# Kernel optimization log

Hardware: AMD Instinct MI355X
Metric: run time of the kernel (lower is better)

## Reference

```python
import jax, jax.numpy as jnp
import numpy as np

T, B, IN, HID, OUT = 512, 2048, 28, 198, 10

def setup_inputs() -> dict:
    key = jax.random.key(0)
    ks = jax.random.split(key, 6)
    s = 1.0 / np.sqrt(HID)
    return {
        "x": jax.random.normal(ks[0], (T, B, IN), dtype=jnp.float32),
        "H": jax.random.normal(ks[1], (HID, HID), dtype=jnp.float32) * s,
        "U": jax.random.normal(ks[2], (IN, HID), dtype=jnp.float32) * s,
        "A": jax.random.normal(ks[3], (OUT, HID), dtype=jnp.float32) * s,
        "b": jax.random.normal(ks[4], (HID,), dtype=jnp.float32) * 0.1,
        "c": jax.random.normal(ks[5], (OUT,), dtype=jnp.float32) * 0.1,
    }

def reference(x, H, U, A, b, c):
    # Precompute input projections for all timesteps in one big GEMM:
    # [T,B,IN] @ [IN,HID] -> [T,B,HID]
    xu = jnp.einsum('tbi,ih->tbh', x, U) + b

    def step(h, xu_t):
        h = jnp.tanh(h @ H.T + xu_t)
        return h, None

    h0 = jnp.zeros((x.shape[1], H.shape[0]), dtype=x.dtype)
    h, _ = jax.lax.scan(step, h0, xu)
    return h @ A.T + c
```

## Files before the change

### kernel.cpp

```cpp
#include <hip/hip_runtime.h>


#define T_STEPS 512
#define BATCH   2048
#define IN_DIM  28
#define HID     198
#define OUT_DIM 10
#define BB      8
#define NTAU    4
#define NTHREADS 1024

typedef __attribute__((ext_vector_type(8))) _Float16 half8;
typedef __attribute__((ext_vector_type(4))) float   floatx4;

__device__ __forceinline__ floatx4 mfma16(half8 a, half8 b, floatx4 c) {
    return __builtin_amdgcn_mfma_f32_16x16x32_f16(a, b, c, 0, 0, 0);
}

__device__ __forceinline__ float fast_tanh(float x) {
    float e = __builtin_amdgcn_exp2f(x * 2.885390081777926357f);
    float r = __builtin_amdgcn_rcpf(e + 1.0f);
    return __builtin_fmaf(-2.0f, r, 1.0f);
}

__device__ __forceinline__ float ror8(float v) {
    return __builtin_bit_cast(float,
        __builtin_amdgcn_mov_dpp(__builtin_bit_cast(int, v),
                                 0x128 , 0xf, 0xf, true));
}

__global__ void __launch_bounds__(NTHREADS, 4)
rnn_kernel(const float* __restrict__ x, const float* __restrict__ H,
           const float* __restrict__ U, const float* __restrict__ A,
           const float* __restrict__ bvec, const float* __restrict__ cvec,
           float* __restrict__ out)
{
    __shared__ __align__(16) _Float16 lds_A[2][NTAU][64][8];
    __shared__ float lds_h[BB][204];

    const int tid  = threadIdx.x;
    const int lane = tid & 63;
    const int wv   = tid >> 6;
    const int n16  = lane & 15;
    const int q    = lane >> 4;
    const int b0   = blockIdx.x * BB;

    {
        _Float16* p0 = &lds_A[0][0][0][0];
        for (int i = tid; i < 2*NTAU*64*8; i += NTHREADS) p0[i] = (_Float16)0.0f;
    }

    const floatx4 zero4 = {0.0f, 0.0f, 0.0f, 0.0f};
    const bool is_cw = (wv < 13);

    const int aslot = lane;

    const int jbase0 = wv*16;
    const int jbase1 = wv*16 + 8;
    const bool g1_on = is_cw && (jbase1 < HID);
    const int jl = n16 & 7;
    const int j0 = jbase0 + jl;
    const int j1 = jbase1 + jl;
    const int b_lane = 2*q + (n16 >> 3);

    half8 Bf0[NTAU], Bf1[NTAU];
    float bias0 = 0.0f, bias1 = 0.0f;
    if (is_cw) {
        bias0 = (n16 < 8 && j0 < HID) ? bvec[j0] : 0.0f;
        bias1 = (n16 < 8 && g1_on)    ? bvec[j1] : 0.0f;
        #pragma unroll
        for (int tau = 0; tau < NTAU; ++tau) {
            half8 f0, f1;
            #pragma unroll
            for (int i = 0; i < 8; ++i) {
                const int k = tau*64 + (n16 >> 3)*32 + q*8 + i;
                float v0 = 0.0f, v1 = 0.0f;
                if (j0 < HID) {
                    if (k < HID)                          v0 = H[j0*HID + k];
                    else if (k >= 224 && k < 224+IN_DIM)  v0 = U[(k-224)*HID + j0];
                }
                if (g1_on) {
                    if (k < HID)                          v1 = H[j1*HID + k];
                    else if (k >= 224 && k < 224+IN_DIM)  v1 = U[(k-224)*HID + j1];
                }
                f0[i] = (_Float16)v0;
                f1[i] = (_Float16)v1;
            }
            Bf0[tau] = f0; Bf1[tau] = f1;
        }
    }

    const int e0_tau  = j0 >> 6;
    const int e0_slot = ((j0 >> 3) & 3)*16 + (b_lane >> 1)*4 + (b_lane & 1)*2
                      + ((j0 >> 5) & 1);
    const int e0_idx  = j0 & 7;
    const int e1_tau  = j1 >> 6;
    const int e1_slot = ((j1 >> 3) & 3)*16 + (b_lane >> 1)*4 + (b_lane & 1)*2
                      + ((j1 >> 5) & 1);
    const int e1_idx  = j1 & 7;

    const int srow = lane & 31, sq = srow >> 3, sr8 = srow & 7;
    const int sslot = sq*16 + (sr8 >> 1)*4 + (sr8 & 1)*2 + 1;
    const float* xrow_s = x + (size_t)(b0 + sr8) * IN_DIM + sq*8;
    const size_t tstride = (size_t)BATCH * IN_DIM;
    floatx4 sA0 = zero4, sA1 = zero4, sB0 = zero4, sB1 = zero4;

    auto issueLd = [&](int tn, floatx4& f0, floatx4& f1) {
        const float* p = xrow_s + (size_t)tn * tstride;
        f0 = *(const floatx4*)p;
        f1 = (sq < 3) ? *(const floatx4*)(p + 4) : zero4;
    };
    auto commitX = [&](floatx4 f0, floatx4 f1, int buf) {
        half8 ax;
        ax[0] = (_Float16)f0[0]; ax[1] = (_Float16)f0[1];
        ax[2] = (_Float16)f0[2]; ax[3] = (_Float16)f0[3];
        ax[4] = (_Float16)f1[0]; ax[5] = (_Float16)f1[1];
        ax[6] = (_Float16)f1[2]; ax[7] = (_Float16)f1[3];
        *(half8*)&lds_A[buf][3][sslot][0] = ax;
    };

    __syncthreads();

    if (wv == 15 && lane < 32) {
        floatx4 t0, t1;
        issueLd(0, t0, t1);
        issueLd(1, sA0, sA1);
        issueLd(2, sB0, sB1);
        commitX(t0, t1, 0);
    }

    auto computeStep = [&](int rb, int wb, bool last) {
        if (!is_cw) return;
        floatx4 a0 = {bias0, bias0, bias0, bias0};
        floatx4 a1 = {bias1, bias1, bias1, bias1};
        #pragma unroll
        for (int tau = 0; tau < NTAU; ++tau) {
            const half8 av = *(const half8*)&lds_A[rb][tau][aslot][0];
            a0 = mfma16(av, Bf0[tau], a0);
            if (g1_on) a1 = mfma16(av, Bf1[tau], a1);
        }
        const float send0 = (n16 < 8) ? a0[2] : a0[1];
        const float send1 = (n16 < 8) ? a1[2] : a1[1];
        const float recv0 = ror8(send0);
        const float recv1 = ror8(send1);
        const float s0 = ((n16 < 8) ? a0[0] : a0[3]) + recv0;
        const float s1 = ((n16 < 8) ? a1[0] : a1[3]) + recv1;
        if (j0 < HID) {
            const float v = fast_tanh(s0);
            lds_A[wb][e0_tau][e0_slot][e0_idx] = (_Float16)v;
            if (last) lds_h[b_lane][j0] = v;
        }
        if (g1_on) {
            const float v = fast_tanh(s1);
            lds_A[wb][e1_tau][e1_slot][e1_idx] = (_Float16)v;
            if (last) lds_h[b_lane][j1] = v;
        }
    };

    #pragma unroll 1
    for (int t = 0; t < T_STEPS; t += 2) {
        __syncthreads();
        if (wv == 15 && lane < 32) {
            commitX(sA0, sA1, 1);
            const int tn = (t+3 < T_STEPS) ? (t+3) : (T_STEPS-1);
            issueLd(tn, sA0, sA1);
        }
        computeStep(0, 1, false);

        __syncthreads();
        if (wv == 15 && lane < 32) {
            commitX(sB0, sB1, 0);
            const int tn = (t+4 < T_STEPS) ? (t+4) : (T_STEPS-1);
            issueLd(tn, sB0, sB1);
        }
        computeStep(1, 0, (t + 2) == T_STEPS);
    }

    __syncthreads();

    if (tid < BB * OUT_DIM) {
        const int r = tid / OUT_DIM;
        const int o = tid % OUT_DIM;
        float s = cvec[o];
        for (int k = 0; k < HID; ++k) s += lds_h[r][k] * A[o*HID + k];
        out[(size_t)(b0 + r) * OUT_DIM + o] = s;
    }
}

extern "C" void kernel_launch(void* const* d_in, const int* in_sizes, int n_in,
                              void* d_out, int out_size, void* d_ws, size_t ws_size,
                              hipStream_t stream) {
    const float* x  = (const float*)d_in[0];
    const float* H  = (const float*)d_in[1];
    const float* U  = (const float*)d_in[2];
    const float* A  = (const float*)d_in[3];
    const float* b  = (const float*)d_in[4];
    const float* c  = (const float*)d_in[5];
    float* out = (float*)d_out;

    rnn_kernel<<<dim3(BATCH / BB), dim3(NTHREADS), 0, stream>>>(x, H, U, A, b, c, out);
}
```

Before: 405.0 us.

## Halve batch tile to 4 rows and spread 3-4 column groups per wave

Each block now handles 4 batch rows with 512 threads instead of 8 rows with 1024. Seven compute waves each own 3 or 4 column groups of 8 and reuse one set of LDS A-fragment loads across those groups. The shared-memory activation layout is shrunk to 32 slots, so half of each MFMA's rows are padding. This doubles the grid to 512 blocks and cuts barrier participants per recurrence step, at the cost of a longer serial MFMA chain per wave and more registers for weights.

```diff
diff --git a/kernel.cpp b/kernel.cpp
--- a/kernel.cpp
+++ b/kernel.cpp
@@ -6,9 +6,10 @@
 #define IN_DIM  28
 #define HID     198
 #define OUT_DIM 10
-#define BB      8
+#define BB      4
 #define NTAU    4
-#define NTHREADS 1024
+#define NTHREADS 512
+#define NGMAX   4
 
 typedef __attribute__((ext_vector_type(8))) _Float16 half8;
 typedef __attribute__((ext_vector_type(4))) float   floatx4;
@@ -35,7 +36,7 @@
            const float* __restrict__ bvec, const float* __restrict__ cvec,
            float* __restrict__ out)
 {
-    __shared__ __align__(16) _Float16 lds_A[2][NTAU][64][8];
+    __shared__ __align__(16) _Float16 lds_A[2][NTAU][32][8];
     __shared__ float lds_h[BB][204];
 
     const int tid  = threadIdx.x;
@@ -43,72 +44,68 @@
     const int wv   = tid >> 6;
     const int n16  = lane & 15;
     const int q    = lane >> 4;
+    const int jl   = n16 & 7;
     const int b0   = blockIdx.x * BB;
 
     {
         _Float16* p0 = &lds_A[0][0][0][0];
-        for (int i = tid; i < 2*NTAU*64*8; i += NTHREADS) p0[i] = (_Float16)0.0f;
+        for (int i = tid; i < 2*NTAU*32*8; i += NTHREADS) p0[i] = (_Float16)0.0f;
     }
 
     const floatx4 zero4 = {0.0f, 0.0f, 0.0f, 0.0f};
-    const bool is_cw = (wv < 13);
+    const bool is_cw = (wv < 7);
 
-    const int aslot = lane;
+    const int aslot = q*8 + (n16 & 7);
 
-    const int jbase0 = wv*16;
-    const int jbase1 = wv*16 + 8;
-    const bool g1_on = is_cw && (jbase1 < HID);
-    const int jl = n16 & 7;
-    const int j0 = jbase0 + jl;
-    const int j1 = jbase1 + jl;
-    const int b_lane = 2*q + (n16 >> 3);
+    const int ng    = (wv < 4) ? 4 : 3;
+    const int gbase = (wv < 4) ? 4*wv : 16 + 3*(wv - 4);
 
-    half8 Bf0[NTAU], Bf1[NTAU];
-    float bias0 = 0.0f, bias1 = 0.0f;
+    const int b_lane = (2*q + (n16 >> 3)) & 3;
+
+    half8 Bf[NGMAX][NTAU];
+    float bias[NGMAX];
+    int   eoff[NGMAX];
+    int   jcol[NGMAX];
     if (is_cw) {
-        bias0 = (n16 < 8 && j0 < HID) ? bvec[j0] : 0.0f;
-        bias1 = (n16 < 8 && g1_on)    ? bvec[j1] : 0.0f;
         #pragma unroll
-        for (int tau = 0; tau < NTAU; ++tau) {
-            half8 f0, f1;
+        for (int g = 0; g < NGMAX; ++g) {
+            const int jbase = (gbase + g) * 8;
+            const int j = jbase + jl;
+            jcol[g] = j;
+            const bool act = (g < ng) && (j < HID);
+            bias[g] = act ? bvec[j] : 0.0f;
+            eoff[g] = (j >> 6)*256
+                    + ((((j >> 3) & 3)*8) + b_lane*2 + ((j >> 5) & 1))*8
+                    + (j & 7);
             #pragma unroll
-            for (int i = 0; i < 8; ++i) {
-                const int k = tau*64 + (n16 >> 3)*32 + q*8 + i;
-                float v0 = 0.0f, v1 = 0.0f;
-                if (j0 < HID) {
-                    if (k < HID)                          v0 = H[j0*HID + k];
-                    else if (k >= 224 && k < 224+IN_DIM)  v0 = U[(k-224)*HID + j0];
+            for (int tau = 0; tau < NTAU; ++tau) {
+                half8 f;
+                #pragma unroll
+                for (int i = 0; i < 8; ++i) {
+                    const int k = tau*64 + (n16 >> 3)*32 + q*8 + i;
+                    float v = 0.0f;
+                    if (act) {
+                        if (k < HID)                          v = H[j*HID + k];
+                        else if (k >= 224 && k < 224+IN_DIM)  v = U[(k-224)*HID + j];
+                    }
+                    f[i] = (_Float16)v;
                 }
-                if (g1_on) {
-                    if (k < HID)                          v1 = H[j1*HID + k];
-                    else if (k >= 224 && k < 224+IN_DIM)  v1 = U[(k-224)*HID + j1];
-                }
-                f0[i] = (_Float16)v0;
-                f1[i] = (_Float16)v1;
+                Bf[g][tau] = f;
             }
-            Bf0[tau] = f0; Bf1[tau] = f1;
         }
     }
 
-    const int e0_tau  = j0 >> 6;
-    const int e0_slot = ((j0 >> 3) & 3)*16 + (b_lane >> 1)*4 + (b_lane & 1)*2
-                      + ((j0 >> 5) & 1);
-    const int e0_idx  = j0 & 7;
-    const int e1_tau  = j1 >> 6;
-    const int e1_slot = ((j1 >> 3) & 3)*16 + (b_lane >> 1)*4 + (b_lane & 1)*2
-                      + ((j1 >> 5) & 1);
-    const int e1_idx  = j1 & 7;
-
-    const int srow = lane & 31, sq = srow >> 3, sr8 = srow & 7;
-    const int sslot = sq*16 + (sr8 >> 1)*4 + (sr8 & 1)*2 + 1;
-    const float* xrow_s = x + (size_t)(b0 + sr8) * IN_DIM + sq*8;
+    const int sb  = (lane >> 2) & 3;
+    const int skq = lane & 3;
+    const int sslot = skq*8 + sb*2 + 1;
+    const float* xrow_s = x + (size_t)(b0 + sb) * IN_DIM + skq*8;
     const size_t tstride = (size_t)BATCH * IN_DIM;
     floatx4 sA0 = zero4, sA1 = zero4, sB0 = zero4, sB1 = zero4;
 
     auto issueLd = [&](int tn, floatx4& f0, floatx4& f1) {
         const float* p = xrow_s + (size_t)tn * tstride;
         f0 = *(const floatx4*)p;
-        f1 = (sq < 3) ? *(const floatx4*)(p + 4) : zero4;
+        f1 = (skq < 3) ? *(const floatx4*)(p + 4) : zero4;
     };
     auto commitX = [&](floatx4 f0, floatx4 f1, int buf) {
         half8 ax;
@@ -121,7 +118,7 @@
 
     __syncthreads();
 
-    if (wv == 15 && lane < 32) {
+    if (wv == 7 && lane < 16) {
         floatx4 t0, t1;
         issueLd(0, t0, t1);
         issueLd(1, sA0, sA1);
@@ -131,36 +128,34 @@
 
     auto computeStep = [&](int rb, int wb, bool last) {
         if (!is_cw) return;
-        floatx4 a0 = {bias0, bias0, bias0, bias0};
-        floatx4 a1 = {bias1, bias1, bias1, bias1};
+        half8 av[NTAU];
         #pragma unroll
-        for (int tau = 0; tau < NTAU; ++tau) {
-            const half8 av = *(const half8*)&lds_A[rb][tau][aslot][0];
-            a0 = mfma16(av, Bf0[tau], a0);
-            if (g1_on) a1 = mfma16(av, Bf1[tau], a1);
-        }
-        const float send0 = (n16 < 8) ? a0[2] : a0[1];
-        const float send1 = (n16 < 8) ? a1[2] : a1[1];
-        const float recv0 = ror8(send0);
-        const float recv1 = ror8(send1);
-        const float s0 = ((n16 < 8) ? a0[0] : a0[3]) + recv0;
-        const float s1 = ((n16 < 8) ? a1[0] : a1[3]) + recv1;
-        if (j0 < HID) {
-            const float v = fast_tanh(s0);
-            lds_A[wb][e0_tau][e0_slot][e0_idx] = (_Float16)v;
-            if (last) lds_h[b_lane][j0] = v;
-        }
-        if (g1_on) {
-            const float v = fast_tanh(s1);
-            lds_A[wb][e1_tau][e1_slot][e1_idx] = (_Float16)v;
-            if (last) lds_h[b_lane][j1] = v;
+        for (int tau = 0; tau < NTAU; ++tau)
+            av[tau] = *(const half8*)&lds_A[rb][tau][aslot][0];
+        _Float16* wbase = &lds_A[wb][0][0][0];
+        #pragma unroll
+        for (int g = 0; g < NGMAX; ++g) {
+            if (g < ng) {
+                floatx4 a = {bias[g], 0.0f, 0.0f, bias[g]};
+                #pragma unroll
+                for (int tau = 0; tau < NTAU; ++tau)
+                    a = mfma16(av[tau], Bf[g][tau], a);
+                const float send = (n16 < 8) ? a[2] : a[1];
+                const float recv = ror8(send);
+                const float s = ((n16 < 8) ? a[0] : a[3]) + recv;
+                const float v = fast_tanh(s);
+                if (q < 2 && jcol[g] < HID) {
+                    wbase[eoff[g]] = (_Float16)v;
+                    if (last) lds_h[b_lane][jcol[g]] = v;
+                }
+            }
         }
     };
 
     #pragma unroll 1
     for (int t = 0; t < T_STEPS; t += 2) {
         __syncthreads();
-        if (wv == 15 && lane < 32) {
+        if (wv == 7 && lane < 16) {
             commitX(sA0, sA1, 1);
             const int tn = (t+3 < T_STEPS) ? (t+3) : (T_STEPS-1);
             issueLd(tn, sA0, sA1);
@@ -168,7 +163,7 @@
         computeStep(0, 1, false);
 
         __syncthreads();
-        if (wv == 15 && lane < 32) {
+        if (wv == 7 && lane < 16) {
             commitX(sB0, sB1, 0);
             const int tn = (t+4 < T_STEPS) ? (t+4) : (T_STEPS-1);
             issueLd(tn, sB0, sB1);
```

New measurement: 532.5 us. 31.5% more time.

## Replace per-step block barriers with LDS flag counters for producer/consumer sync

Applied to the files above, without the earlier changes.

Replaces the two __syncthreads per timestep pair with workgroup-scope atomic counters in shared memory. Compute waves spin until the four groups writing the read buffer have signalled, and the x-loader wave has committed its slice. They signal once their reads of a buffer finish, so writers wait only for readers of the target buffer, not for the whole block. This lets waves drift apart and hides barrier latency, but adds spin-wait polling on LDS and relies on the counter protocol and memory ordering being correct.

```diff
diff --git a/kernel.cpp b/kernel.cpp
--- a/kernel.cpp
+++ b/kernel.cpp
@@ -9,6 +9,7 @@
 #define BB      8
 #define NTAU    4
 #define NTHREADS 1024
+#define NCW     13
 
 typedef __attribute__((ext_vector_type(8))) _Float16 half8;
 typedef __attribute__((ext_vector_type(4))) float   floatx4;
@@ -27,6 +28,15 @@
     return __builtin_bit_cast(float,
         __builtin_amdgcn_mov_dpp(__builtin_bit_cast(int, v),
                                  0x128 , 0xf, 0xf, true));
+}
+
+__device__ __forceinline__ void spin_ge(unsigned* f, unsigned target) {
+    while (__hip_atomic_load(f, __ATOMIC_ACQUIRE,
+                             __HIP_MEMORY_SCOPE_WORKGROUP) < target) { }
+}
+__device__ __forceinline__ void signal_add(unsigned* f) {
+    __hip_atomic_fetch_add(f, 1u, __ATOMIC_RELEASE,
+                           __HIP_MEMORY_SCOPE_WORKGROUP);
 }
 
 __global__ void __launch_bounds__(NTHREADS, 4)
@@ -37,6 +47,7 @@
 {
     __shared__ __align__(16) _Float16 lds_A[2][NTAU][64][8];
     __shared__ float lds_h[BB][204];
+    __shared__ unsigned s_flags[10];
 
     const int tid  = threadIdx.x;
     const int lane = tid & 63;
@@ -49,9 +60,14 @@
         _Float16* p0 = &lds_A[0][0][0][0];
         for (int i = tid; i < 2*NTAU*64*8; i += NTHREADS) p0[i] = (_Float16)0.0f;
     }
+    if (tid == 0) {
+        s_flags[0] = 4; s_flags[1] = 4; s_flags[2] = 4; s_flags[3] = 1;
+        s_flags[4] = 0; s_flags[5] = 0; s_flags[6] = 0; s_flags[7] = 0;
+        s_flags[8] = 0; s_flags[9] = 0;
+    }
 
     const floatx4 zero4 = {0.0f, 0.0f, 0.0f, 0.0f};
-    const bool is_cw = (wv < 13);
+    const bool is_cw = (wv < NCW);
 
     const int aslot = lane;
 
@@ -121,59 +137,86 @@
 
     __syncthreads();
 
-    if (wv == 15 && lane < 32) {
-        floatx4 t0, t1;
-        issueLd(0, t0, t1);
-        issueLd(1, sA0, sA1);
-        issueLd(2, sB0, sB1);
-        commitX(t0, t1, 0);
-    }
-
-    auto computeStep = [&](int rb, int wb, bool last) {
+    if (wv == 15) {
+        if (lane < 32) {
+            floatx4 t0, t1;
+            issueLd(0, t0, t1);
+            issueLd(1, sA0, sA1);
+            issueLd(2, sB0, sB1);
+            commitX(t0, t1, 0);
+        }
+        if (lane == 0) signal_add(&s_flags[3]);
+    }
+
+    auto computeStep = [&](int rb, int wb, bool last, unsigned np, unsigned nrw) {
         if (!is_cw) return;
+        spin_ge(&s_flags[rb*4+0], 4u*np);
+        spin_ge(&s_flags[rb*4+1], 4u*np);
+        spin_ge(&s_flags[rb*4+2], 4u*np);
+        spin_ge(&s_flags[rb*4+3], 2u*np);
+        half8 av[NTAU];
+        #pragma unroll
+        for (int tau = 0; tau < NTAU; ++tau)
+            av[tau] = *(const half8*)&lds_A[rb][tau][aslot][0];
         floatx4 a0 = {bias0, bias0, bias0, bias0};
         floatx4 a1 = {bias1, bias1, bias1, bias1};
         #pragma unroll
         for (int tau = 0; tau < NTAU; ++tau) {
-            const half8 av = *(const half8*)&lds_A[rb][tau][aslot][0];
-            a0 = mfma16(av, Bf0[tau], a0);
-            if (g1_on) a1 = mfma16(av, Bf1[tau], a1);
-        }
+            a0 = mfma16(av[tau], Bf0[tau], a0);
+            if (g1_on) a1 = mfma16(av[tau], Bf1[tau], a1);
+        }
+        if (lane == 0) signal_add(&s_flags[8+rb]);
         const float send0 = (n16 < 8) ? a0[2] : a0[1];
         const float send1 = (n16 < 8) ? a1[2] : a1[1];
         const float recv0 = ror8(send0);
         const float recv1 = ror8(send1);
         const float s0 = ((n16 < 8) ? a0[0] : a0[3]) + recv0;
         const float s1 = ((n16 < 8) ? a1[0] : a1[3]) + recv1;
+        const float v0 = fast_tanh(s0);
+        const float v1 = fast_tanh(s1);
+        spin_ge(&s_flags[8+wb], 13u*nrw);
         if (j0 < HID) {
-            const float v = fast_tanh(s0);
-            lds_A[wb][e0_tau][e0_slot][e0_idx] = (_Float16)v;
-            if (last) lds_h[b_lane][j0] = v;
+            lds_A[wb][e0_tau][e0_slot][e0_idx] = (_Float16)v0;
+            if (last) lds_h[b_lane][j0] = v0;
         }
         if (g1_on) {
-            const float v = fast_tanh(s1);
-            lds_A[wb][e1_tau][e1_slot][e1_idx] = (_Float16)v;
-            if (last) lds_h[b_lane][j1] = v;
-        }
+            lds_A[wb][e1_tau][e1_slot][e1_idx] = (_Float16)v1;
+            if (last) lds_h[b_lane][j1] = v1;
+        }
+        if (lane == 0) signal_add(&s_flags[wb*4 + (wv >> 2)]);
     };
 
+    unsigned np0 = 1, np1 = 1;
+    unsigned nr0 = 1, nr1 = 0;
     #pragma unroll 1
     for (int t = 0; t < T_STEPS; t += 2) {
-        __syncthreads();
-        if (wv == 15 && lane < 32) {
-            commitX(sA0, sA1, 1);
-            const int tn = (t+3 < T_STEPS) ? (t+3) : (T_STEPS-1);
-            issueLd(tn, sA0, sA1);
-        }
-        computeStep(0, 1, false);
-
-        __syncthreads();
-        if (wv == 15 && lane < 32) {
-            commitX(sB0, sB1, 0);
-            const int tn = (t+4 < T_STEPS) ? (t+4) : (T_STEPS-1);
-            issueLd(tn, sB0, sB1);
-        }
-        computeStep(1, 0, (t + 2) == T_STEPS);
+        if (wv == 15) {
+            if (lane < 32) {
+                spin_ge(&s_flags[9], 13u*nr1);
+                commitX(sA0, sA1, 1);
+            }
+            if (lane == 0) signal_add(&s_flags[4+3]);
+            if (lane < 32) {
+                const int tn = (t+3 < T_STEPS) ? (t+3) : (T_STEPS-1);
+                issueLd(tn, sA0, sA1);
+            }
+        }
+        computeStep(0, 1, false, np0, nr1);
+        np0 += 1; nr1 += 1;
+
+        if (wv == 15) {
+            if (lane < 32) {
+                spin_ge(&s_flags[8], 13u*nr0);
+                commitX(sB0, sB1, 0);
+            }
+            if (lane == 0) signal_add(&s_flags[0+3]);
+            if (lane < 32) {
+                const int tn = (t+4 < T_STEPS) ? (t+4) : (T_STEPS-1);
+                issueLd(tn, sB0, sB1);
+            }
+        }
+        computeStep(1, 0, (t + 2) == T_STEPS, np1, nr0);
+        np1 += 1; nr0 += 1;
     }
 
     __syncthreads();
```

New measurement: 456.0 us. +12.6%, slower.
